# Kernel optimization log

Measured on AMD Instinct MI355X. Metric: run time of the kernel, lower is better.

The kernel has to match this reference:

```python
import jax, jax.numpy as jnp
import numpy as np

N_NODES = 50000
N_EDGES = 600000
IN_CH = 128
HID = 128
OUT_CH = 16
N_REL = 8
NEG_SLOPE = 0.2


def glorot(key, shape):
    fan_in, fan_out = shape[-2], shape[-1]
    lim = (6.0 / (fan_in + fan_out)) ** 0.5
    return jax.random.uniform(key, shape, jnp.float32, -lim, lim)


def setup_inputs() -> dict:
    key = jax.random.key(0)
    ks = jax.random.split(key, 16)
    x = jax.random.normal(ks[0], (N_NODES, IN_CH), jnp.float32)
    edge_index = jax.random.randint(ks[1], (2, N_EDGES), 0, N_NODES, jnp.int64)
    edge_type = jax.random.randint(ks[2], (N_EDGES,), 0, N_REL, jnp.int64)
    return {
        "x": x,
        "W1": glorot(ks[3], (N_REL, IN_CH, HID)),
        "q1": glorot(ks[4], (HID, 1)),
        "k1": glorot(ks[5], (HID, 1)),
        "b1": jnp.zeros((HID,), jnp.float32),
        "W2": glorot(ks[6], (N_REL, HID, HID)),
        "q2": glorot(ks[7], (HID, 1)),
        "k2": glorot(ks[8], (HID, 1)),
        "b2": jnp.zeros((HID,), jnp.float32),
        "lin_w": glorot(ks[9], (HID, OUT_CH)),
        "lin_b": jnp.zeros((OUT_CH,), jnp.float32),
        "edge_index": edge_index,
        "edge_type": edge_type,
    }


def rgat_conv(x, W, q, k, b, src, dst, etype, n_nodes):
    # Per-relation linear transform of all nodes: [R, N, H]
    xw = jnp.einsum('ni,rio->rno', x, W)
    hj = xw[etype, src]  # transformed source features per edge [E, H]
    hi = xw[etype, dst]  # transformed target features per edge [E, H]
    # additive self-attention logits (heads=1, dim=1): [E, 1]
    a = jax.nn.leaky_relu(hi @ q + hj @ k, NEG_SLOPE)
    # segment softmax over incoming edges of each target node (across-relation)
    amax = jax.ops.segment_max(a, dst, num_segments=n_nodes)  # [N, 1]
    e = jnp.exp(a - amax[dst])
    denom = jax.ops.segment_sum(e, dst, num_segments=n_nodes)  # [N, 1]
    alpha = e / denom[dst]
    # weighted scatter-add aggregation + bias
    out = jax.ops.segment_sum(alpha * hj, dst, num_segments=n_nodes)
    return out + b


def reference(x, W1, q1, k1, b1, W2, q2, k2, b2, lin_w, lin_b, edge_index, edge_type):
    src, dst = edge_index[0], edge_index[1]
    n = x.shape[0]
    h = jax.nn.relu(rgat_conv(x, W1, q1, k1, b1, src, dst, edge_type, n))
    h = jax.nn.relu(rgat_conv(h, W2, q2, k2, b2, src, dst, edge_type, n))
    h = h @ lin_w + lin_b                 # [N, out]
    g = jnp.mean(h, axis=0, keepdims=True)  # global_mean_pool -> [1, out]
    return jax.nn.log_softmax(g, axis=-1)
```

## Files before the change

kernel.cpp:

```cpp
#include <hip/hip_runtime.h>

#define CH 128
#define N_REL 8
#define OUT_CH 16
#define NEG_SLOPE 0.2f

typedef short short8 __attribute__((ext_vector_type(8)));
typedef float f32x4 __attribute__((ext_vector_type(4)));

__device__ __forceinline__ unsigned short f2bf(float f) {
    unsigned u = __float_as_uint(f);
    return (unsigned short)((u + 0x7fffu + ((u >> 16) & 1u)) >> 16);
}


__device__ __forceinline__ void dev_cast(const float* __restrict__ X,
                                         unsigned short* __restrict__ Xb,
                                         long total, int b, int tid) {
    long i = ((long)b * 256 + tid) * 8;
    if (i >= total) return;
    float4 v0 = *(const float4*)(X + i);
    float4 v1 = *(const float4*)(X + i + 4);
    ushort4 a, c;
    a.x = f2bf(v0.x); a.y = f2bf(v0.y); a.z = f2bf(v0.z); a.w = f2bf(v0.w);
    c.x = f2bf(v1.x); c.y = f2bf(v1.y); c.z = f2bf(v1.z); c.w = f2bf(v1.w);
    *(ushort4*)(Xb + i) = a;
    *(ushort4*)(Xb + i + 4) = c;
}

__device__ __forceinline__ void dev_wqk(const float* __restrict__ W,
                                        const float* __restrict__ qv,
                                        const float* __restrict__ kv,
                                        float* __restrict__ wq, float* __restrict__ wk,
                                        int rb, int tid) {
    int r = rb * 2 + (tid >> 7);
    int i = tid & 127;
    const float* row = W + ((size_t)r * CH + i) * CH;
    float aq = 0.f, ak = 0.f;
    for (int o = 0; o < CH; ++o) { float w = row[o]; aq += w * qv[o]; ak += w * kv[o]; }
    wq[r * CH + i] = aq;
    wk[r * CH + i] = ak;
}

__device__ __forceinline__ void dev_wpack(const float* __restrict__ W,
                                          unsigned short* __restrict__ Wpk, int t) {
    int lane = t & 63, ks = (t >> 6) & 3, ct = (t >> 8) & 7, r = t >> 11;
    int l15 = lane & 15, g = lane >> 4;
    const float* src = W + ((size_t)r * CH + ks * 32 + g * 8) * CH + ct * 16 + l15;
    unsigned pk[4];
    #pragma unroll
    for (int p = 0; p < 4; ++p) {
        unsigned lo = f2bf(src[(2 * p) * CH]);
        unsigned hi = f2bf(src[(2 * p + 1) * CH]);
        pk[p] = lo | (hi << 16);
    }
    *(uint4*)(Wpk + (size_t)t * 8) = make_uint4(pk[0], pk[1], pk[2], pk[3]);
}

__device__ __forceinline__ void dev_qkpack(const float* __restrict__ wq,
                                           const float* __restrict__ wk,
                                           unsigned short* __restrict__ qkf, int tid) {
    int lane = tid & 63, ks = tid >> 6;
    int j = lane & 15, g = lane >> 4;
    const float* col = (j < 8) ? (wq + j * CH) : (wk + (j - 8) * CH);
    int k0 = ks * 32 + g * 8;
    unsigned pk[4];
    #pragma unroll
    for (int p = 0; p < 4; ++p) {
        unsigned lo = f2bf(col[k0 + 2 * p]);
        unsigned hi = f2bf(col[k0 + 2 * p + 1]);
        pk[p] = lo | (hi << 16);
    }
    *(uint4*)(qkf + (size_t)tid * 8) = make_uint4(pk[0], pk[1], pk[2], pk[3]);
}


__global__ void k_cast_hist(const float* __restrict__ X, unsigned short* __restrict__ Xb,
                            long total, const int* __restrict__ dst,
                            int* __restrict__ count, int ne, int nb_cast) {
    int b = blockIdx.x, tid = threadIdx.x;
    if (b < nb_cast) {
        dev_cast(X, Xb, total, b, tid);
    } else {
        int e = (b - nb_cast) * 256 + tid;
        if (e < ne) atomicAdd(count + dst[e], 1);
    }
}

__global__ __launch_bounds__(256) void k_scan1_wqk(const int* __restrict__ count,
                                                   int* __restrict__ rowptr,
                                                   int* __restrict__ bsum, int n, int nbscan,
                                                   const float* __restrict__ W,
                                                   const float* __restrict__ qv,
                                                   const float* __restrict__ kv,
                                                   float* __restrict__ wq,
                                                   float* __restrict__ wk) {
    int b = blockIdx.x, tid = threadIdx.x;
    if (b >= nbscan) { dev_wqk(W, qv, kv, wq, wk, b - nbscan, tid); return; }
    __shared__ int wsum[4];
    int lane = tid & 63, w = tid >> 6;
    int i0 = b * 1024 + tid * 4;
    int v0 = 0, v1 = 0, v2 = 0, v3 = 0;
    if (i0 + 3 < n) {
        int4 v = *(const int4*)(count + i0);
        v0 = v.x; v1 = v.y; v2 = v.z; v3 = v.w;
    } else {
        if (i0 < n) v0 = count[i0];
        if (i0 + 1 < n) v1 = count[i0 + 1];
        if (i0 + 2 < n) v2 = count[i0 + 2];
        if (i0 + 3 < n) v3 = count[i0 + 3];
    }
    int t1 = v0 + v1, t2 = t1 + v2, t3 = t2 + v3;
    int s = t3;
    #pragma unroll
    for (int off = 1; off < 64; off <<= 1) {
        int t = __shfl_up(s, off);
        if (lane >= off) s += t;
    }
    if (lane == 63) wsum[w] = s;
    __syncthreads();
    int wpre = 0;
    #pragma unroll
    for (int i = 0; i < 4; ++i) wpre += (i < w) ? wsum[i] : 0;
    int excl = wpre + s - t3;
    if (i0 < n) rowptr[i0] = excl;
    if (i0 + 1 < n) rowptr[i0 + 1] = excl + v0;
    if (i0 + 2 < n) rowptr[i0 + 2] = excl + t1;
    if (i0 + 3 < n) rowptr[i0 + 3] = excl + t2;
    if (tid == 0) bsum[b] = wsum[0] + wsum[1] + wsum[2] + wsum[3];
}

__global__ __launch_bounds__(256) void k_scan2_wprep(int* __restrict__ bsum,
                                                     int* __restrict__ total, int nb,
                                                     const float* __restrict__ W,
                                                     unsigned short* __restrict__ Wpk,
                                                     const float* __restrict__ wq,
                                                     const float* __restrict__ wk,
                                                     unsigned short* __restrict__ qkf) {
    int b = blockIdx.x, tid = threadIdx.x;
    if (b == 0) {
        if (tid >= 64) return;
        int lane = tid;
        int carry = 0;
        for (int base = 0; base < nb; base += 64) {
            int i = base + lane;
            int v = (i < nb) ? bsum[i] : 0;
            int s = v;
            #pragma unroll
            for (int off = 1; off < 64; off <<= 1) {
                int t = __shfl_up(s, off);
                if (lane >= off) s += t;
            }
            if (i < nb) bsum[i] = carry + s - v;
            carry += __shfl(s, 63);
        }
        if (lane == 0) *total = carry;
    } else if (b <= 64) {
        dev_wpack(W, Wpk, (b - 1) * 256 + tid);
    } else {
        dev_qkpack(wq, wk, qkf, tid);
    }
}

__global__ __launch_bounds__(256) void k_scan3(int* __restrict__ rowptr,
                                               int* __restrict__ rowptr_work,
                                               const int* __restrict__ bsum,
                                               const int* __restrict__ total, int n) {
    int b = blockIdx.x;
    int i0 = b * 1024 + threadIdx.x * 4;
    int add = bsum[b];
    #pragma unroll
    for (int j = 0; j < 4; ++j) {
        int i = i0 + j;
        if (i < n) {
            int v = rowptr[i] + add;
            rowptr[i] = v;
            rowptr_work[i] = v;
        }
    }
    if (b == 0 && threadIdx.x == 0) rowptr[n] = *total;
}


__global__ __launch_bounds__(256, 1) void k_fat(
    const unsigned short* __restrict__ Xb, const unsigned short* __restrict__ Wpk,
    const unsigned short* __restrict__ qkf, unsigned short* __restrict__ XW,
    float* __restrict__ sq, float* __restrict__ sk, int n, int nwaves,
    int nb_gemm, int nb_sqsk,
    const int* __restrict__ esrc, const int* __restrict__ edst,
    const int* __restrict__ etp, int* __restrict__ rowptr_work,
    int* __restrict__ pe, int ne) {
    const int b = blockIdx.x, tid = threadIdx.x;
    const int wv = tid >> 6, lane = tid & 63;
    const int l15 = lane & 15, g = lane >> 4;
    const int ntiles = (n + 15) >> 4;

    if (b < nb_gemm) {
        const int w = b * 4 + wv;
        const int r = w & 7;
        const int slot = w >> 3;
        const int nslots = nwaves >> 3;

        short8 wf[8][4];
        const unsigned short* wr = Wpk + ((size_t)r * 32 * 64 + lane) * 8;
        #pragma unroll
        for (int ct = 0; ct < 8; ++ct)
            #pragma unroll
            for (int ks = 0; ks < 4; ++ks) {
                wf[ct][ks] = *(const short8*)(wr + (size_t)(ct * 4 + ks) * 64 * 8);
                asm volatile("" : "+v"(wf[ct][ks]));
            }

        for (int t = slot; t < ntiles; t += nslots) {
            int row = t * 16 + l15;
            bool ok = row < n;
            int rowc = ok ? row : n - 1;
            const unsigned short* xrow = Xb + (size_t)rowc * CH + g * 8;
            short8 xf[4];
            #pragma unroll
            for (int ks = 0; ks < 4; ++ks) xf[ks] = *(const short8*)(xrow + ks * 32);
            unsigned short* orow = XW + ((size_t)r * n + row) * CH;
            #pragma unroll
            for (int ct = 0; ct < 8; ++ct) {
                f32x4 a = {0.f, 0.f, 0.f, 0.f};
                #pragma unroll
                for (int ks = 0; ks < 4; ++ks)
                    a = __builtin_amdgcn_mfma_f32_16x16x32_bf16(wf[ct][ks], xf[ks], a, 0, 0, 0);
                unsigned p01, p23;
                asm("v_cvt_pk_bf16_f32 %0, %1, %2" : "=v"(p01) : "v"(a[0]), "v"(a[1]));
                asm("v_cvt_pk_bf16_f32 %0, %1, %2" : "=v"(p23) : "v"(a[2]), "v"(a[3]));
                if (ok) *(uint2*)(orow + ct * 16 + g * 4) = make_uint2(p01, p23);
            }
        }
    } else if (b < nb_gemm + nb_sqsk) {
        const int t = (b - nb_gemm) * 4 + wv;
        if (t >= ntiles) return;
        short8 qf[4];
        #pragma unroll
        for (int ks = 0; ks < 4; ++ks)
            qf[ks] = *(const short8*)(qkf + (size_t)(ks * 64 + lane) * 8);
        int row = t * 16 + l15;
        bool ok = row < n;
        int rowc = ok ? row : n - 1;
        const unsigned short* xrow = Xb + (size_t)rowc * CH + g * 8;
        short8 xf[4];
        #pragma unroll
        for (int ks = 0; ks < 4; ++ks) xf[ks] = *(const short8*)(xrow + ks * 32);
        f32x4 dq = {0.f, 0.f, 0.f, 0.f};
        #pragma unroll
        for (int ks = 0; ks < 4; ++ks)
            dq = __builtin_amdgcn_mfma_f32_16x16x32_bf16(qf[ks], xf[ks], dq, 0, 0, 0);
        if (ok) {
            float* base = (g < 2) ? sq : sk;
            int j0 = (g & 1) * 4;
            #pragma unroll
            for (int reg = 0; reg < 4; ++reg)
                base[(size_t)(j0 + reg) * n + row] = dq[reg];
        }
    } else {
        int e = (b - nb_gemm - nb_sqsk) * 256 + tid;
        if (e >= ne) return;
        int pos = atomicAdd(rowptr_work + edst[e], 1);
        pe[pos] = (esrc[e] & 0xffff) | (etp[e] << 16);
    }
}


__global__ __launch_bounds__(256) void k_attn_wqk(
    const int* __restrict__ rowptr, const int* __restrict__ pe,
    const float* __restrict__ sq, const float* __restrict__ sk,
    const unsigned short* __restrict__ XW, const float* __restrict__ bias,
    unsigned short* __restrict__ outb, int n_nodes,
    const float* __restrict__ Wn, const float* __restrict__ qn,
    const float* __restrict__ kn, float* __restrict__ wqn,
    float* __restrict__ wkn, int nb_wqk) {
    int b = blockIdx.x;
    if (b < nb_wqk) { dev_wqk(Wn, qn, kn, wqn, wkn, b, threadIdx.x); return; }
    int wid = ((b - nb_wqk) * 256 + threadIdx.x) >> 6;
    int lane = threadIdx.x & 63;
    if (wid >= n_nodes) return;
    const int l16 = lane & 15, g16 = lane >> 4;
    int r0 = rowptr[wid], r1 = rowptr[wid + 1];
    float acc[8] = {};
    float denom = 0.f;

    if (r1 > r0) {
        float sqv = (lane < N_REL) ? sq[lane * n_nodes + wid] : 0.f;

        float m = -1e30f;
        for (int c0 = r0; c0 < r1; c0 += 64) {
            int j = c0 + lane;
            float a = -1e30f;
            if (j < r1) {
                int p = pe[j];
                int s = p & 0xffff, t = p >> 16;
                float av = __shfl(sqv, t) + sk[t * n_nodes + s];
                a = av >= 0.f ? av : NEG_SLOPE * av;
            }
            m = fmaxf(m, a);
        }
        #pragma unroll
        for (int off = 32; off; off >>= 1) m = fmaxf(m, __shfl_xor(m, off));

        for (int c0 = r0; c0 < r1; c0 += 64) {
            int j = c0 + lane;
            float ev = 0.f;
            int p = 0;
            if (j < r1) {
                p = pe[j];
                int s = p & 0xffff, t = p >> 16;
                float av = __shfl(sqv, t) + sk[t * n_nodes + s];
                av = av >= 0.f ? av : NEG_SLOPE * av;
                ev = __expf(av - m);
            }
            float evs = ev;
            #pragma unroll
            for (int off = 32; off; off >>= 1) evs += __shfl_xor(evs, off);
            denom += evs;

            int C = r1 - c0;
            if (C > 64) C = 64;
            for (int jj = 0; jj < C; jj += 4) {
                int lsel = jj + g16;
                float evj = __shfl(ev, lsel);
                int pj = __shfl(p, lsel);
                int s = pj & 0xffff, t = pj >> 16;
                const unsigned short* row = XW + ((size_t)(t * n_nodes + s)) * CH + l16 * 8;
                uint4 v = *(const uint4*)row;
                acc[0] += evj * __uint_as_float(v.x << 16);
                acc[1] += evj * __uint_as_float(v.x & 0xffff0000u);
                acc[2] += evj * __uint_as_float(v.y << 16);
                acc[3] += evj * __uint_as_float(v.y & 0xffff0000u);
                acc[4] += evj * __uint_as_float(v.z << 16);
                acc[5] += evj * __uint_as_float(v.z & 0xffff0000u);
                acc[6] += evj * __uint_as_float(v.w << 16);
                acc[7] += evj * __uint_as_float(v.w & 0xffff0000u);
            }
        }
    }

    #pragma unroll
    for (int i = 0; i < 8; ++i) {
        acc[i] += __shfl_xor(acc[i], 16);
        acc[i] += __shfl_xor(acc[i], 32);
    }

    if (lane < 16) {
        float inv = denom > 0.f ? 1.f / denom : 0.f;
        unsigned pk[4];
        #pragma unroll
        for (int i = 0; i < 4; ++i) {
            float b0 = bias[l16 * 8 + 2 * i];
            float b1 = bias[l16 * 8 + 2 * i + 1];
            float o0 = acc[2 * i] * inv + b0;
            float o1 = acc[2 * i + 1] * inv + b1;
            o0 = o0 > 0.f ? o0 : 0.f;
            o1 = o1 > 0.f ? o1 : 0.f;
            pk[i] = (unsigned)f2bf(o0) | ((unsigned)f2bf(o1) << 16);
        }
        *(uint4*)(outb + (size_t)wid * CH + l16 * 8) = make_uint4(pk[0], pk[1], pk[2], pk[3]);
    }
}


__global__ __launch_bounds__(256) void k_wprep2(const float* __restrict__ W,
                                                unsigned short* __restrict__ Wpk,
                                                const float* __restrict__ wq,
                                                const float* __restrict__ wk,
                                                unsigned short* __restrict__ qkf) {
    int b = blockIdx.x, tid = threadIdx.x;
    if (b < 64) dev_wpack(W, Wpk, b * 256 + tid);
    else dev_qkpack(wq, wk, qkf, tid);
}


__global__ __launch_bounds__(256) void k_colsum(const unsigned short* __restrict__ h,
                                                float* __restrict__ sum, int n_nodes) {
    __shared__ float cs[CH];
    int tid = threadIdx.x;
    int c2 = (tid & 63) * 2;
    int rw = tid >> 6;
    if (tid < CH) cs[tid] = 0.f;
    __syncthreads();
    float a0 = 0.f, a1 = 0.f;
    for (int row = blockIdx.x * 4 + rw; row < n_nodes; row += gridDim.x * 4) {
        unsigned v = *(const unsigned*)(h + (size_t)row * CH + c2);
        a0 += __uint_as_float(v << 16);
        a1 += __uint_as_float(v & 0xffff0000u);
    }
    atomicAdd(&cs[c2], a0);
    atomicAdd(&cs[c2 + 1], a1);
    __syncthreads();
    if (tid < CH) atomicAdd(sum + tid, cs[tid]);
}

__global__ void k_head(const float* __restrict__ sum, const float* __restrict__ lw,
                       const float* __restrict__ lb, float* __restrict__ outp, int n_nodes) {
    __shared__ float mean[CH];
    int t = threadIdx.x;
    mean[t] = sum[t] / (float)n_nodes;
    __syncthreads();
    if (t < OUT_CH) {
        float g = lb[t];
        for (int i = 0; i < CH; ++i) g += mean[i] * lw[i * OUT_CH + t];
        float m = g;
        #pragma unroll
        for (int off = 8; off; off >>= 1) m = fmaxf(m, __shfl_xor(m, off, 16));
        float ex = expf(g - m);
        float se = ex;
        #pragma unroll
        for (int off = 8; off; off >>= 1) se += __shfl_xor(se, off, 16);
        outp[t] = g - m - logf(se);
    }
}

extern "C" void kernel_launch(void* const* d_in, const int* in_sizes, int n_in,
                              void* d_out, int out_size, void* d_ws, size_t ws_size,
                              hipStream_t stream) {
    const float* x  = (const float*)d_in[0];
    const float* W1 = (const float*)d_in[1];
    const float* q1 = (const float*)d_in[2];
    const float* k1 = (const float*)d_in[3];
    const float* b1 = (const float*)d_in[4];
    const float* W2 = (const float*)d_in[5];
    const float* q2 = (const float*)d_in[6];
    const float* k2 = (const float*)d_in[7];
    const float* b2 = (const float*)d_in[8];
    const float* lw = (const float*)d_in[9];
    const float* lb = (const float*)d_in[10];
    const int* ei   = (const int*)d_in[11];
    const int* etp  = (const int*)d_in[12];

    const int n  = in_sizes[0] / CH;
    const int ne = in_sizes[12];
    const int* esrc = ei;
    const int* edst = ei + ne;

    char* ws = (char*)d_ws;
    size_t off = 0;
    auto carve = [&](size_t bytes) -> char* {
        char* p = ws + off;
        off = (off + bytes + 255) & ~(size_t)255;
        return p;
    };
    unsigned short* xw  = (unsigned short*)carve((size_t)N_REL * n * CH * 2);
    unsigned short* xb  = (unsigned short*)carve((size_t)n * CH * 2);
    unsigned short* h1b = (unsigned short*)carve((size_t)n * CH * 2);
    unsigned short* h2b = (unsigned short*)carve((size_t)n * CH * 2);
    unsigned short* wpk = (unsigned short*)carve((size_t)N_REL * 32 * 64 * 8 * 2);
    unsigned short* qkf = (unsigned short*)carve((size_t)256 * 8 * 2);
    float* sq     = (float*)carve((size_t)N_REL * n * 4);
    float* sk     = (float*)carve((size_t)N_REL * n * 4);
    float* wq     = (float*)carve(N_REL * CH * 4);
    float* wk     = (float*)carve(N_REL * CH * 4);
    int* count    = (int*)carve((size_t)n * 4);
    int* rowptr   = (int*)carve((size_t)(n + 1) * 4);
    int* rowptr_w = (int*)carve((size_t)n * 4);
    int* pe       = (int*)carve((size_t)ne * 4);
    int* bsum     = (int*)carve((size_t)256 * 4);
    int* total    = (int*)carve(4);
    float* sum128 = (float*)carve(CH * 4);

    hipMemsetAsync(count, 0, (size_t)n * 4, stream);
    hipMemsetAsync(sum128, 0, CH * 4, stream);

    const int nbscan = (n + 1023) / 1024;
    const int nb_cast = (int)(((long)n * CH / 8 + 255) / 256);
    const int nb_hist = (ne + 255) / 256;
    const int NW = 2048;
    const int nb_gemm = NW / 4;
    const int ntiles = (n + 15) >> 4;
    const int nb_sqsk = (ntiles + 3) / 4;
    const int nb_scat = (ne + 255) / 256;
    const int nb_attn = (n + 3) / 4;

    k_cast_hist<<<nb_cast + nb_hist, 256, 0, stream>>>(x, xb, (long)n * CH, edst, count, ne, nb_cast);
    k_scan1_wqk<<<nbscan + 4, 256, 0, stream>>>(count, rowptr, bsum, n, nbscan, W1, q1, k1, wq, wk);
    k_scan2_wprep<<<66, 256, 0, stream>>>(bsum, total, nbscan, W1, wpk, wq, wk, qkf);
    k_scan3<<<nbscan, 256, 0, stream>>>(rowptr, rowptr_w, bsum, total, n);
    k_fat<<<nb_gemm + nb_sqsk + nb_scat, 256, 0, stream>>>(xb, wpk, qkf, xw, sq, sk, n, NW,
                                                           nb_gemm, nb_sqsk,
                                                           esrc, edst, etp, rowptr_w, pe, ne);
    k_attn_wqk<<<4 + nb_attn, 256, 0, stream>>>(rowptr, pe, sq, sk, xw, b1, h1b, n,
                                                W2, q2, k2, wq, wk, 4);
    k_wprep2<<<65, 256, 0, stream>>>(W2, wpk, wq, wk, qkf);
    k_fat<<<nb_gemm + nb_sqsk, 256, 0, stream>>>(h1b, wpk, qkf, xw, sq, sk, n, NW,
                                                 nb_gemm, nb_sqsk,
                                                 esrc, edst, etp, rowptr_w, pe, 0);
    k_attn_wqk<<<nb_attn, 256, 0, stream>>>(rowptr, pe, sq, sk, xw, b2, h2b, n,
                                            (const float*)nullptr, (const float*)nullptr,
                                            (const float*)nullptr, (float*)nullptr,
                                            (float*)nullptr, 0);

    k_colsum<<<256, 256, 0, stream>>>(h2b, sum128, n);
    k_head<<<1, CH, 0, stream>>>(sum128, lw, lb, (float*)d_out, n);
}
```

Before: 248.0 us.

## Stage per-relation GEMM weights in LDS instead of registers in k_fat

The weight fragments for each relation are now loaded cooperatively into a 32 KB shared-memory buffer per block and read from LDS inside the MFMA loop, instead of being pinned in 128 VGPRs per lane. Each block now serves a single relation, and the launch-bounds minimum-blocks hint is dropped, so register pressure falls and more waves can be resident. The trade-off is extra LDS reads in the inner loop and a block-wide barrier. The 32 KB LDS allocation also applies to the sqsk and scatter blocks that share this kernel, which may cap their occupancy.

```diff
diff --git a/kernel.cpp b/kernel.cpp
--- a/kernel.cpp
+++ b/kernel.cpp
@@ -182,36 +182,34 @@
 }
 
 
-__global__ __launch_bounds__(256, 1) void k_fat(
+__global__ __launch_bounds__(256) void k_fat(
     const unsigned short* __restrict__ Xb, const unsigned short* __restrict__ Wpk,
     const unsigned short* __restrict__ qkf, unsigned short* __restrict__ XW,
-    float* __restrict__ sq, float* __restrict__ sk, int n, int nwaves,
+    float* __restrict__ sq, float* __restrict__ sk, int n,
     int nb_gemm, int nb_sqsk,
     const int* __restrict__ esrc, const int* __restrict__ edst,
     const int* __restrict__ etp, int* __restrict__ rowptr_work,
     int* __restrict__ pe, int ne) {
+    __shared__ unsigned short lds_w[32 * 64 * 8];
     const int b = blockIdx.x, tid = threadIdx.x;
     const int wv = tid >> 6, lane = tid & 63;
     const int l15 = lane & 15, g = lane >> 4;
     const int ntiles = (n + 15) >> 4;
 
     if (b < nb_gemm) {
-        const int w = b * 4 + wv;
-        const int r = w & 7;
-        const int slot = w >> 3;
-        const int nslots = nwaves >> 3;
-
-        short8 wf[8][4];
-        const unsigned short* wr = Wpk + ((size_t)r * 32 * 64 + lane) * 8;
-        #pragma unroll
-        for (int ct = 0; ct < 8; ++ct)
-            #pragma unroll
-            for (int ks = 0; ks < 4; ++ks) {
-                wf[ct][ks] = *(const short8*)(wr + (size_t)(ct * 4 + ks) * 64 * 8);
-                asm volatile("" : "+v"(wf[ct][ks]));
-            }
-
-        for (int t = slot; t < ntiles; t += nslots) {
+        const int r = b & 7;
+        const int nslots = (nb_gemm >> 3) * 4;
+        const int slot0 = (b >> 3) * 4 + wv;
+
+        const unsigned short* wsrc = Wpk + (size_t)r * 32 * 64 * 8;
+        #pragma unroll
+        for (int i = 0; i < 8; ++i) {
+            int idx = tid + i * 256;
+            *(uint4*)(lds_w + idx * 8) = *(const uint4*)(wsrc + (size_t)idx * 8);
+        }
+        __syncthreads();
+
+        for (int t = slot0; t < ntiles; t += nslots) {
             int row = t * 16 + l15;
             bool ok = row < n;
             int rowc = ok ? row : n - 1;
@@ -224,8 +222,10 @@
             for (int ct = 0; ct < 8; ++ct) {
                 f32x4 a = {0.f, 0.f, 0.f, 0.f};
                 #pragma unroll
-                for (int ks = 0; ks < 4; ++ks)
-                    a = __builtin_amdgcn_mfma_f32_16x16x32_bf16(wf[ct][ks], xf[ks], a, 0, 0, 0);
+                for (int ks = 0; ks < 4; ++ks) {
+                    short8 wf = *(const short8*)(lds_w + ((ct * 4 + ks) * 64 + lane) * 8);
+                    a = __builtin_amdgcn_mfma_f32_16x16x32_bf16(wf, xf[ks], a, 0, 0, 0);
+                }
                 unsigned p01, p23;
                 asm("v_cvt_pk_bf16_f32 %0, %1, %2" : "=v"(p01) : "v"(a[0]), "v"(a[1]));
                 asm("v_cvt_pk_bf16_f32 %0, %1, %2" : "=v"(p23) : "v"(a[2]), "v"(a[3]));
@@ -467,8 +467,7 @@
     const int nbscan = (n + 1023) / 1024;
     const int nb_cast = (int)(((long)n * CH / 8 + 255) / 256);
     const int nb_hist = (ne + 255) / 256;
-    const int NW = 2048;
-    const int nb_gemm = NW / 4;
+    const int nb_gemm = 512;
     const int ntiles = (n + 15) >> 4;
     const int nb_sqsk = (ntiles + 3) / 4;
     const int nb_scat = (ne + 255) / 256;
@@ -478,13 +477,13 @@
     k_scan1_wqk<<<nbscan + 4, 256, 0, stream>>>(count, rowptr, bsum, n, nbscan, W1, q1, k1, wq, wk);
     k_scan2_wprep<<<66, 256, 0, stream>>>(bsum, total, nbscan, W1, wpk, wq, wk, qkf);
     k_scan3<<<nbscan, 256, 0, stream>>>(rowptr, rowptr_w, bsum, total, n);
-    k_fat<<<nb_gemm + nb_sqsk + nb_scat, 256, 0, stream>>>(xb, wpk, qkf, xw, sq, sk, n, NW,
+    k_fat<<<nb_gemm + nb_sqsk + nb_scat, 256, 0, stream>>>(xb, wpk, qkf, xw, sq, sk, n,
                                                            nb_gemm, nb_sqsk,
                                                            esrc, edst, etp, rowptr_w, pe, ne);
     k_attn_wqk<<<4 + nb_attn, 256, 0, stream>>>(rowptr, pe, sq, sk, xw, b1, h1b, n,
                                                 W2, q2, k2, wq, wk, 4);
     k_wprep2<<<65, 256, 0, stream>>>(W2, wpk, wq, wk, qkf);
-    k_fat<<<nb_gemm + nb_sqsk, 256, 0, stream>>>(h1b, wpk, qkf, xw, sq, sk, n, NW,
+    k_fat<<<nb_gemm + nb_sqsk, 256, 0, stream>>>(h1b, wpk, qkf, xw, sq, sk, n,
                                                  nb_gemm, nb_sqsk,
                                                  esrc, edst, etp, rowptr_w, pe, 0);
     k_attn_wqk<<<nb_attn, 256, 0, stream>>>(rowptr, pe, sq, sk, xw, b2, h2b, n,
```

Measured after the change: 247.2 us. Within noise of the previous version (-0.3%).
